# Optimization experiments

Measured on AMD Instinct MI355X. Metric: run time of the kernel, lower is better.

The kernel has to match this reference:

```python
import jax, jax.numpy as jnp
import numpy as np

B, L, H, KV, D, HID = 2, 2048, 16, 4, 128, 2048
EPS = 1e-6
ROPE_BASE = 10000.0


def _rotate_half(x):
    x1, x2 = jnp.split(x, 2, axis=-1)
    return jnp.concatenate((-x2, x1), axis=-1)


def _rms_norm(x, w):
    xf = x.astype(jnp.float32)
    var = jnp.mean(xf * xf, axis=-1, keepdims=True)
    return w * (xf * jax.lax.rsqrt(var + EPS)).astype(x.dtype)


def setup_inputs() -> dict:
    key = jax.random.key(0)
    ks = jax.random.split(key, 6)
    hidden_states = jax.random.normal(ks[0], (B, L, HID), dtype=jnp.float32)
    # rotary embeddings (standard rope table)
    inv_freq = 1.0 / (ROPE_BASE ** (jnp.arange(0, D, 2, dtype=jnp.float32) / D))
    pos = jnp.arange(L, dtype=jnp.float32)
    freqs = pos[:, None] * inv_freq[None, :]          # [L, D/2]
    emb = jnp.concatenate((freqs, freqs), axis=-1)    # [L, D]
    cos = jnp.broadcast_to(jnp.cos(emb)[None], (B, L, D))
    sin = jnp.broadcast_to(jnp.sin(emb)[None], (B, L, D))
    s = 0.02
    Wq = jax.random.normal(ks[1], (HID, H * D), dtype=jnp.float32) * s
    Wk = jax.random.normal(ks[2], (HID, KV * D), dtype=jnp.float32) * s
    Wv = jax.random.normal(ks[3], (HID, KV * D), dtype=jnp.float32) * s
    Wo = jax.random.normal(ks[4], (H * D, HID), dtype=jnp.float32) * s
    q_norm_w = jnp.ones((D,), dtype=jnp.float32)
    k_norm_w = jnp.ones((D,), dtype=jnp.float32)
    return {"hidden_states": hidden_states, "cos": cos, "sin": sin,
            "Wq": Wq, "Wk": Wk, "Wv": Wv, "Wo": Wo,
            "q_norm_w": q_norm_w, "k_norm_w": k_norm_w}


def reference(hidden_states, cos, sin, Wq, Wk, Wv, Wo, q_norm_w, k_norm_w):
    scale = D ** -0.5
    n_rep = H // KV
    q = (hidden_states @ Wq).reshape(B, L, H, D)
    k = (hidden_states @ Wk).reshape(B, L, KV, D)
    v = (hidden_states @ Wv).reshape(B, L, KV, D)
    q = _rms_norm(q, q_norm_w).transpose(0, 2, 1, 3)   # [B,H,L,D]
    k = _rms_norm(k, k_norm_w).transpose(0, 2, 1, 3)   # [B,KV,L,D]
    v = v.transpose(0, 2, 1, 3)                         # [B,KV,L,D]
    c = cos[:, None]                                    # [B,1,L,D]
    s = sin[:, None]
    q = q * c + _rotate_half(q) * s
    k = k * c + _rotate_half(k) * s
    # GQA without materializing repeated K/V: group query heads per kv head.
    qg = q.reshape(B, KV, n_rep, L, D)
    scores = jnp.einsum('bgrld,bgmd->bgrlm', qg, k) * scale
    attn = jax.nn.softmax(scores, axis=-1)
    out = jnp.einsum('bgrlm,bgmd->bgrld', attn, v)      # [B,KV,n_rep,L,D]
    out = out.reshape(B, H, L, D).transpose(0, 2, 1, 3).reshape(B, L, H * D)
    return out @ Wo
```

## Files before the change

### kernel.cpp

```cpp
#include <hip/hip_runtime.h>

typedef unsigned short u16;
typedef unsigned int u32;
typedef short bf16x8 __attribute__((ext_vector_type(8)));
typedef float f32x4 __attribute__((ext_vector_type(4)));

#define B_ 2
#define L_ 2048
#define H_ 16
#define KV_ 4
#define D_ 128
#define HID_ 2048

#define QSCALE (0.08838834764831845f * 1.4426950408889634f)
#define SMAX 17.0f

__device__ __forceinline__ u16 f2bf(float f) {
  union { float f; u32 u; } v; v.f = f;
  u32 u = v.u;
  return (u16)((u + 0x7FFFu + ((u >> 16) & 1u)) >> 16);
}
__device__ __forceinline__ float bf2f(u16 h) {
  union { u32 u; float f; } v; v.u = ((u32)h) << 16;
  return v.f;
}
__device__ __forceinline__ u32 pkbf(float a, float b) {
  union { float f; u32 u; } x, y; x.f = a; y.f = b;
  return ((x.u + 0x8000u) >> 16) | ((y.u + 0x8000u) & 0xffff0000u);
}
__device__ __forceinline__ void gl_lds16(const void* g, void* l) {
  __builtin_amdgcn_global_load_lds((__attribute__((address_space(1))) void*)(g),
                                   (__attribute__((address_space(3))) void*)(l),
                                   16, 0, 0);
}

__global__ void k_f2b(const float* __restrict__ src, u16* __restrict__ dst, int n4) {
  int i = blockIdx.x * 256 + threadIdx.x;
  if (i >= n4) return;
  float4 v = ((const float4*)src)[i];
  u32 a = (u32)f2bf(v.x) | ((u32)f2bf(v.y) << 16);
  u32 b = (u32)f2bf(v.z) | ((u32)f2bf(v.w) << 16);
  ((uint2*)dst)[i] = make_uint2(a, b);
}

__global__ void k_tconv_all(const float* __restrict__ Wq, const float* __restrict__ Wk,
                            const float* __restrict__ Wv, const float* __restrict__ Wo,
                            u16* __restrict__ Wtqkv, u16* __restrict__ Wto) {
  __shared__ float t[32][33];
  int id = blockIdx.x;
  const float* src; u16* dst; int C; int ct, rt;
  if (id < 4096)      { src = Wq; dst = Wtqkv;               C = 2048; ct = id & 63; rt = id >> 6; }
  else if (id < 5120) { id -= 4096; src = Wk; dst = Wtqkv + 2048 * 2048; C = 512; ct = id & 15; rt = id >> 4; }
  else if (id < 6144) { id -= 5120; src = Wv; dst = Wtqkv + 2560 * 2048; C = 512; ct = id & 15; rt = id >> 4; }
  else                { id -= 6144; src = Wo; dst = Wto;     C = 2048; ct = id & 63; rt = id >> 6; }
  const int R = 2048;
  int c0 = ct * 32, r0 = rt * 32;
  for (int i = threadIdx.y; i < 32; i += 8)
    t[i][threadIdx.x] = src[(size_t)(r0 + i) * C + c0 + threadIdx.x];
  __syncthreads();
  for (int i = threadIdx.y; i < 32; i += 8)
    dst[(size_t)(c0 + i) * R + r0 + threadIdx.x] = f2bf(t[threadIdx.x][i]);
}

template <int OUT_BF16>
__global__ __launch_bounds__(256, 2) void k_gemm_bt(
    const u16* __restrict__ A, const u16* __restrict__ Bt, void* __restrict__ Cv,
    int M, int N, int K) {
  __shared__ u16 smem[16384];
  u16* As = smem;
  u16* Bs = smem + 8192;
  const int tid = threadIdx.x;
  const int wave = tid >> 6, lane = tid & 63;
  const int wr = wave >> 1, wc = wave & 1;
  const int quad = lane >> 4, fm = lane & 15;
  const int m0 = blockIdx.y * 128, n0 = blockIdx.x * 128;
  f32x4 acc[4][4];
  for (int i = 0; i < 4; ++i)
    for (int j = 0; j < 4; ++j)
      for (int r = 0; r < 4; ++r) acc[i][j][r] = 0.0f;

  const int lrow = lane >> 3;
  const int lcol = (lane & 7) * 8;
  const int fk = quad * 8;

  for (int kt = 0; kt < K; kt += 64) {
    for (int p = 0; p < 4; ++p) {
      int roff = wave * 32 + p * 8 + lrow;
      gl_lds16(A + (size_t)(m0 + roff) * K + kt + lcol,
               As + wave * 2048 + p * 512 + lane * 8);
      gl_lds16(Bt + (size_t)(n0 + roff) * K + kt + lcol,
               Bs + wave * 2048 + p * 512 + lane * 8);
    }
    __syncthreads();
    for (int s = 0; s < 2; ++s) {
      bf16x8 af[4], bfr[4];
      for (int i = 0; i < 4; ++i)
        af[i] = *(const bf16x8*)(As + (wr * 64 + i * 16 + fm) * 64 + s * 32 + fk);
      for (int j = 0; j < 4; ++j)
        bfr[j] = *(const bf16x8*)(Bs + (wc * 64 + j * 16 + fm) * 64 + s * 32 + fk);
      for (int i = 0; i < 4; ++i)
        for (int j = 0; j < 4; ++j)
          acc[i][j] = __builtin_amdgcn_mfma_f32_16x16x32_bf16(af[i], bfr[j],
                                                              acc[i][j], 0, 0, 0);
    }
    __syncthreads();
  }

  if (OUT_BF16) {
    u16* Cs = smem;
    for (int hh = 0; hh < 2; ++hh) {
      if (hh) __syncthreads();
      if (wr == hh)
        for (int i = 0; i < 4; ++i)
          for (int j = 0; j < 4; ++j)
            for (int r = 0; r < 4; ++r)
              Cs[(i * 16 + quad * 4 + r) * 136 + wc * 64 + j * 16 + fm] =
                  f2bf(acc[i][j][r]);
      __syncthreads();
      for (int it = 0; it < 4; ++it) {
        int row = it * 16 + (tid >> 4);
        int col = (tid & 15) * 8;
        uint4 v = *(const uint4*)(Cs + row * 136 + col);
        *(uint4*)((u16*)Cv + (size_t)(m0 + hh * 64 + row) * N + n0 + col) = v;
      }
    }
  } else {
    float* Cf = (float*)smem;
    for (int p = 0; p < 4; ++p) {
      if (p) __syncthreads();
      if (wr == (p >> 1))
        for (int ii = 0; ii < 2; ++ii) {
          int i = 2 * (p & 1) + ii;
          for (int j = 0; j < 4; ++j)
            for (int r = 0; r < 4; ++r)
              Cf[(ii * 16 + quad * 4 + r) * 132 + wc * 64 + j * 16 + fm] =
                  acc[i][j][r];
        }
      __syncthreads();
      for (int it = 0; it < 4; ++it) {
        int row = it * 8 + (tid >> 5);
        int col = (tid & 31) * 4;
        float4 v = *(const float4*)(Cf + row * 132 + col);
        *(float4*)((float*)Cv + (size_t)(m0 + p * 32 + row) * N + n0 + col) = v;
      }
    }
  }
}

__global__ __launch_bounds__(256) void k_norm_rope(
    const u16* __restrict__ qkv, const float* __restrict__ cosp,
    const float* __restrict__ sinp, const float* __restrict__ qw,
    const float* __restrict__ kw, u16* __restrict__ Qb, u16* __restrict__ Kb,
    u16* __restrict__ Vtb) {
  int wid = blockIdx.x * 4 + (threadIdx.x >> 6);
  int lane = threadIdx.x & 63;
  int tok = wid / 24, unit = wid % 24;
  int b = tok >> 11, l = tok & 2047;
  const u16* row = qkv + (size_t)tok * 3072;
  int d0 = lane * 2;
  if (unit < 20) {
    int isq = unit < 16;
    int col = isq ? unit * 128 : 2048 + (unit - 16) * 128;
    u32 u = *(const u32*)(row + col + d0);
    float x0 = bf2f((u16)(u & 0xffff)), x1 = bf2f((u16)(u >> 16));
    float ss = x0 * x0 + x1 * x1;
    for (int m = 1; m < 64; m <<= 1) ss += __shfl_xor(ss, m);
    float rr = rsqrtf(ss * (1.0f / 128.0f) + 1e-6f);
    const float* wv = isq ? qw : kw;
    float n0 = x0 * rr * wv[d0], n1 = x1 * rr * wv[d0 + 1];
    float p0 = __shfl_xor(n0, 32), p1 = __shfl_xor(n1, 32);
    float sgn = (lane < 32) ? -1.0f : 1.0f;
    const float* cb = cosp + (size_t)tok * 128;
    const float* sb = sinp + (size_t)tok * 128;
    float o0 = n0 * cb[d0] + sgn * p0 * sb[d0];
    float o1 = n1 * cb[d0 + 1] + sgn * p1 * sb[d0 + 1];
    if (isq) {
      o0 *= QSCALE;
      o1 *= QSCALE;
      u32 packed = (u32)f2bf(o0) | ((u32)f2bf(o1) << 16);
      size_t off = (((size_t)(b * H_ + unit)) * L_ + l) * D_ + d0;
      *(u32*)(Qb + off) = packed;
    } else {
      u32 packed = (u32)f2bf(o0) | ((u32)f2bf(o1) << 16);
      size_t off = (((size_t)(b * KV_ + (unit - 16))) * L_ + l) * D_ + d0;
      *(u32*)(Kb + off) = packed;
    }
  } else {
    int g = unit - 20;
    int lp = (l & ~31) | (((l >> 2) & 3) << 3) | (((l >> 4) & 1) << 2) | (l & 3);
    size_t base = (((size_t)(b * KV_ + g)) * D_ + d0) * L_ + lp;
    Vtb[base] = row[2560 + g * 128 + d0];
    Vtb[base + L_] = row[2560 + g * 128 + d0 + 1];
  }
}

__global__ __launch_bounds__(256, 4) void k_attn(const u16* __restrict__ Qb,
                                                 const u16* __restrict__ Kb,
                                                 const u16* __restrict__ Vtb,
                                                 u16* __restrict__ AO) {
  __shared__ u16 smem[16384];
  u16* Ks = smem;
  u16* Vs = smem + 8192;
  const int tid = threadIdx.x, wave = tid >> 6, lane = tid & 63;
  const int quad = lane >> 4, fm = lane & 15;
  const int f7 = fm & 7;
  const int qt = blockIdx.x, bh = blockIdx.y;
  const int b = bh >> 4, h = bh & 15, g = h >> 2;
  const u16* Kg = Kb + ((size_t)(b * KV_ + g)) * L_ * D_;
  const u16* Vg = Vtb + ((size_t)(b * KV_ + g)) * D_ * L_;

  const u16* Qg = Qb + ((size_t)bh * L_ + qt * 64 + wave * 16 + fm) * D_;
  bf16x8 qf[4];
  for (int ks = 0; ks < 4; ++ks)
    qf[ks] = *(const bf16x8*)(Qg + ks * 32 + quad * 8);

  f32x4 o[8];
  for (int f = 0; f < 8; ++f)
    for (int r = 0; r < 4; ++r) o[f][r] = 0.0f;
  float lrun = 0.0f;

  const int eK = wave * 2048 + (lane << 3);
  const int cK = lane & 15;
  const int cV = lane & 7;
  for (int kt = 0; kt < 32; ++kt) {
    __syncthreads();
    for (int p = 0; p < 4; ++p) {
      int e = eK + p * 512;
      int rowK = e >> 7;
      int gK = (cK & 8) | ((cK & 7) ^ (rowK & 7));
      gl_lds16(Kg + (size_t)(kt * 64 + rowK) * 128 + gK * 8, Ks + e);
      int rowV = e >> 6;
      int gV = cV ^ (rowV & 7);
      gl_lds16(Vg + (size_t)rowV * L_ + kt * 64 + gV * 8, Vs + e);
    }
    __syncthreads();

    f32x4 s[4];
    for (int n = 0; n < 4; ++n)
      for (int r = 0; r < 4; ++r) s[n][r] = 0.0f;
    for (int ks = 0; ks < 4; ++ks) {
      int c = 4 * ks + quad;
      int cp = (c & 8) | ((c & 7) ^ f7);
      for (int n = 0; n < 4; ++n) {
        bf16x8 kf = *(const bf16x8*)(Ks + (n * 16 + fm) * 128 + cp * 8);
        s[n] = __builtin_amdgcn_mfma_f32_16x16x32_bf16(kf, qf[ks], s[n], 0, 0, 0);
      }
    }

    u32 pk[4][2];
    float rs = 0.0f;
    for (int n = 0; n < 4; ++n) {
      float p0 = __builtin_amdgcn_exp2f(s[n][0] - SMAX);
      float p1 = __builtin_amdgcn_exp2f(s[n][1] - SMAX);
      float p2 = __builtin_amdgcn_exp2f(s[n][2] - SMAX);
      float p3 = __builtin_amdgcn_exp2f(s[n][3] - SMAX);
      rs += (p0 + p1) + (p2 + p3);
      pk[n][0] = pkbf(p0, p1);
      pk[n][1] = pkbf(p2, p3);
    }
    lrun += rs;

    for (int ks2 = 0; ks2 < 2; ++ks2) {
      union { u32 u[4]; bf16x8 v; } pa;
      pa.u[0] = pk[2 * ks2][0];
      pa.u[1] = pk[2 * ks2][1];
      pa.u[2] = pk[2 * ks2 + 1][0];
      pa.u[3] = pk[2 * ks2 + 1][1];
      int chunk = (4 * ks2 + quad) ^ f7;
      for (int f = 0; f < 8; ++f) {
        bf16x8 vv = *(const bf16x8*)(Vs + (f * 16 + fm) * 64 + chunk * 8);
        o[f] = __builtin_amdgcn_mfma_f32_16x16x32_bf16(pa.v, vv, o[f], 0, 0, 0);
      }
    }
  }

  lrun += __shfl_xor(lrun, 16);
  lrun += __shfl_xor(lrun, 32);
  float li = 1.0f / lrun;
  float l0 = __shfl(li, (lane & 48) | (quad * 4 + 0));
  float l1 = __shfl(li, (lane & 48) | (quad * 4 + 1));
  float l2 = __shfl(li, (lane & 48) | (quad * 4 + 2));
  float l3 = __shfl(li, (lane & 48) | (quad * 4 + 3));
  __syncthreads();
  for (int f = 0; f < 8; ++f) {
    int e = (wave * 16 + quad * 4) * 136 + f * 16 + fm;
    smem[e] = f2bf(o[f][0] * l0);
    smem[e + 136] = f2bf(o[f][1] * l1);
    smem[e + 272] = f2bf(o[f][2] * l2);
    smem[e + 408] = f2bf(o[f][3] * l3);
  }
  __syncthreads();
  const size_t tok0 = (size_t)b * L_ + qt * 64;
  for (int it = 0; it < 8; ++it) {
    int rrow = wave * 16 + it * 2 + (lane >> 5);
    int cc = (lane & 31) * 4;
    uint2 v = *(const uint2*)(smem + rrow * 136 + cc);
    *(uint2*)(AO + (tok0 + rrow) * (H_ * D_) + h * D_ + cc) = v;
  }
}

extern "C" void kernel_launch(void* const* d_in, const int* in_sizes, int n_in,
                              void* d_out, int out_size, void* d_ws,
                              size_t ws_size, hipStream_t stream) {
  const float* hidden = (const float*)d_in[0];
  const float* cosp = (const float*)d_in[1];
  const float* sinp = (const float*)d_in[2];
  const float* Wq = (const float*)d_in[3];
  const float* Wk = (const float*)d_in[4];
  const float* Wv = (const float*)d_in[5];
  const float* Wo = (const float*)d_in[6];
  const float* qw = (const float*)d_in[7];
  const float* kw = (const float*)d_in[8];
  float* out = (float*)d_out;

  char* w = (char*)d_ws;
  u16* Xb = (u16*)(w);
  u16* Wtqkv = (u16*)(w + (16u << 20));
  u16* Wto = (u16*)(w + (28u << 20));
  u16* qkv = (u16*)(w + (36u << 20));
  u16* Qb = (u16*)(w + (60u << 20));
  u16* Kb = (u16*)(w + (76u << 20));
  u16* Vtb = (u16*)(w + (80u << 20));
  u16* AO = Xb;

  k_f2b<<<8192, 256, 0, stream>>>(hidden, Xb, 2097152);
  k_tconv_all<<<10240, dim3(32, 8), 0, stream>>>(Wq, Wk, Wv, Wo, Wtqkv, Wto);
  k_gemm_bt<1><<<dim3(24, 32), 256, 0, stream>>>(Xb, Wtqkv, qkv, 4096, 3072, 2048);
  k_norm_rope<<<24576, 256, 0, stream>>>(qkv, cosp, sinp, qw, kw, Qb, Kb, Vtb);
  k_attn<<<dim3(32, 32), 256, 0, stream>>>(Qb, Kb, Vtb, AO);
  k_gemm_bt<0><<<dim3(16, 32), 256, 0, stream>>>(AO, Wto, out, 4096, 2048, 2048);
}
```

Measured before the change: 363.7 us.

## Process two 16-row query tiles per wave in attention to reuse K/V fragments

The attention kernel now gives each wave 32 query rows split into two independent accumulator sets. Each K and V fragment read from LDS feeds two MFMAs instead of one, and each block's K/V tile load serves 128 queries instead of 64. This halves the attention grid and lowers occupancy, with launch bounds moved from 4 to 2 blocks to make room for the doubled registers. The QKV/output GEMM launch bounds also change from 2 to 3 blocks per CU, which may force more register pressure or spilling.

```diff
diff --git a/kernel.cpp b/kernel.cpp
--- a/kernel.cpp
+++ b/kernel.cpp
@@ -63,7 +63,7 @@
 }
 
 template <int OUT_BF16>
-__global__ __launch_bounds__(256, 2) void k_gemm_bt(
+__global__ __launch_bounds__(256, 3) void k_gemm_bt(
     const u16* __restrict__ A, const u16* __restrict__ Bt, void* __restrict__ Cv,
     int M, int N, int K) {
   __shared__ u16 smem[16384];
@@ -194,7 +194,7 @@
   }
 }
 
-__global__ __launch_bounds__(256, 4) void k_attn(const u16* __restrict__ Qb,
+__global__ __launch_bounds__(256, 2) void k_attn(const u16* __restrict__ Qb,
                                                  const u16* __restrict__ Kb,
                                                  const u16* __restrict__ Vtb,
                                                  u16* __restrict__ AO) {
@@ -209,15 +209,17 @@
   const u16* Kg = Kb + ((size_t)(b * KV_ + g)) * L_ * D_;
   const u16* Vg = Vtb + ((size_t)(b * KV_ + g)) * D_ * L_;
 
-  const u16* Qg = Qb + ((size_t)bh * L_ + qt * 64 + wave * 16 + fm) * D_;
-  bf16x8 qf[4];
-  for (int ks = 0; ks < 4; ++ks)
-    qf[ks] = *(const bf16x8*)(Qg + ks * 32 + quad * 8);
-
-  f32x4 o[8];
+  const u16* Qg = Qb + ((size_t)bh * L_ + qt * 128 + wave * 32 + fm) * D_;
+  bf16x8 qf1[4], qf2[4];
+  for (int ks = 0; ks < 4; ++ks) {
+    qf1[ks] = *(const bf16x8*)(Qg + ks * 32 + quad * 8);
+    qf2[ks] = *(const bf16x8*)(Qg + 16 * D_ + ks * 32 + quad * 8);
+  }
+
+  f32x4 o1[8], o2[8];
   for (int f = 0; f < 8; ++f)
-    for (int r = 0; r < 4; ++r) o[f][r] = 0.0f;
-  float lrun = 0.0f;
+    for (int r = 0; r < 4; ++r) { o1[f][r] = 0.0f; o2[f][r] = 0.0f; }
+  float lr1 = 0.0f, lr2 = 0.0f;
 
   const int eK = wave * 2048 + (lane << 3);
   const int cK = lane & 15;
@@ -235,67 +237,86 @@
     }
     __syncthreads();
 
-    f32x4 s[4];
+    f32x4 s1[4], s2[4];
     for (int n = 0; n < 4; ++n)
-      for (int r = 0; r < 4; ++r) s[n][r] = 0.0f;
+      for (int r = 0; r < 4; ++r) { s1[n][r] = 0.0f; s2[n][r] = 0.0f; }
     for (int ks = 0; ks < 4; ++ks) {
       int c = 4 * ks + quad;
       int cp = (c & 8) | ((c & 7) ^ f7);
       for (int n = 0; n < 4; ++n) {
         bf16x8 kf = *(const bf16x8*)(Ks + (n * 16 + fm) * 128 + cp * 8);
-        s[n] = __builtin_amdgcn_mfma_f32_16x16x32_bf16(kf, qf[ks], s[n], 0, 0, 0);
+        s1[n] = __builtin_amdgcn_mfma_f32_16x16x32_bf16(kf, qf1[ks], s1[n], 0, 0, 0);
+        s2[n] = __builtin_amdgcn_mfma_f32_16x16x32_bf16(kf, qf2[ks], s2[n], 0, 0, 0);
       }
     }
 
-    u32 pk[4][2];
-    float rs = 0.0f;
+    u32 pk1[4][2], pk2[4][2];
+    float rs1 = 0.0f, rs2 = 0.0f;
     for (int n = 0; n < 4; ++n) {
-      float p0 = __builtin_amdgcn_exp2f(s[n][0] - SMAX);
-      float p1 = __builtin_amdgcn_exp2f(s[n][1] - SMAX);
-      float p2 = __builtin_amdgcn_exp2f(s[n][2] - SMAX);
-      float p3 = __builtin_amdgcn_exp2f(s[n][3] - SMAX);
-      rs += (p0 + p1) + (p2 + p3);
-      pk[n][0] = pkbf(p0, p1);
-      pk[n][1] = pkbf(p2, p3);
-    }
-    lrun += rs;
+      float a0 = __builtin_amdgcn_exp2f(s1[n][0] - SMAX);
+      float a1 = __builtin_amdgcn_exp2f(s1[n][1] - SMAX);
+      float a2 = __builtin_amdgcn_exp2f(s1[n][2] - SMAX);
+      float a3 = __builtin_amdgcn_exp2f(s1[n][3] - SMAX);
+      rs1 += (a0 + a1) + (a2 + a3);
+      pk1[n][0] = pkbf(a0, a1);
+      pk1[n][1] = pkbf(a2, a3);
+      float b0 = __builtin_amdgcn_exp2f(s2[n][0] - SMAX);
+      float b1 = __builtin_amdgcn_exp2f(s2[n][1] - SMAX);
+      float b2 = __builtin_amdgcn_exp2f(s2[n][2] - SMAX);
+      float b3 = __builtin_amdgcn_exp2f(s2[n][3] - SMAX);
+      rs2 += (b0 + b1) + (b2 + b3);
+      pk2[n][0] = pkbf(b0, b1);
+      pk2[n][1] = pkbf(b2, b3);
+    }
+    lr1 += rs1;
+    lr2 += rs2;
 
     for (int ks2 = 0; ks2 < 2; ++ks2) {
-      union { u32 u[4]; bf16x8 v; } pa;
-      pa.u[0] = pk[2 * ks2][0];
-      pa.u[1] = pk[2 * ks2][1];
-      pa.u[2] = pk[2 * ks2 + 1][0];
-      pa.u[3] = pk[2 * ks2 + 1][1];
+      union { u32 u[4]; bf16x8 v; } pa1, pa2;
+      pa1.u[0] = pk1[2 * ks2][0];
+      pa1.u[1] = pk1[2 * ks2][1];
+      pa1.u[2] = pk1[2 * ks2 + 1][0];
+      pa1.u[3] = pk1[2 * ks2 + 1][1];
+      pa2.u[0] = pk2[2 * ks2][0];
+      pa2.u[1] = pk2[2 * ks2][1];
+      pa2.u[2] = pk2[2 * ks2 + 1][0];
+      pa2.u[3] = pk2[2 * ks2 + 1][1];
       int chunk = (4 * ks2 + quad) ^ f7;
       for (int f = 0; f < 8; ++f) {
         bf16x8 vv = *(const bf16x8*)(Vs + (f * 16 + fm) * 64 + chunk * 8);
-        o[f] = __builtin_amdgcn_mfma_f32_16x16x32_bf16(pa.v, vv, o[f], 0, 0, 0);
+        o1[f] = __builtin_amdgcn_mfma_f32_16x16x32_bf16(pa1.v, vv, o1[f], 0, 0, 0);
+        o2[f] = __builtin_amdgcn_mfma_f32_16x16x32_bf16(pa2.v, vv, o2[f], 0, 0, 0);
       }
     }
   }
 
-  lrun += __shfl_xor(lrun, 16);
-  lrun += __shfl_xor(lrun, 32);
-  float li = 1.0f / lrun;
-  float l0 = __shfl(li, (lane & 48) | (quad * 4 + 0));
-  float l1 = __shfl(li, (lane & 48) | (quad * 4 + 1));
-  float l2 = __shfl(li, (lane & 48) | (quad * 4 + 2));
-  float l3 = __shfl(li, (lane & 48) | (quad * 4 + 3));
-  __syncthreads();
-  for (int f = 0; f < 8; ++f) {
-    int e = (wave * 16 + quad * 4) * 136 + f * 16 + fm;
-    smem[e] = f2bf(o[f][0] * l0);
-    smem[e + 136] = f2bf(o[f][1] * l1);
-    smem[e + 272] = f2bf(o[f][2] * l2);
-    smem[e + 408] = f2bf(o[f][3] * l3);
-  }
-  __syncthreads();
-  const size_t tok0 = (size_t)b * L_ + qt * 64;
-  for (int it = 0; it < 8; ++it) {
-    int rrow = wave * 16 + it * 2 + (lane >> 5);
-    int cc = (lane & 31) * 4;
-    uint2 v = *(const uint2*)(smem + rrow * 136 + cc);
-    *(uint2*)(AO + (tok0 + rrow) * (H_ * D_) + h * D_ + cc) = v;
+  const size_t tok0 = (size_t)b * L_ + qt * 128;
+  for (int grp = 0; grp < 2; ++grp) {
+    f32x4* o = grp ? o2 : o1;
+    float lr = grp ? lr2 : lr1;
+    lr += __shfl_xor(lr, 16);
+    lr += __shfl_xor(lr, 32);
+    float li = 1.0f / lr;
+    float l0 = __shfl(li, (lane & 48) | (quad * 4 + 0));
+    float l1 = __shfl(li, (lane & 48) | (quad * 4 + 1));
+    float l2 = __shfl(li, (lane & 48) | (quad * 4 + 2));
+    float l3 = __shfl(li, (lane & 48) | (quad * 4 + 3));
+    __syncthreads();
+    for (int f = 0; f < 8; ++f) {
+      int e = (wave * 16 + quad * 4) * 136 + f * 16 + fm;
+      smem[e] = f2bf(o[f][0] * l0);
+      smem[e + 136] = f2bf(o[f][1] * l1);
+      smem[e + 272] = f2bf(o[f][2] * l2);
+      smem[e + 408] = f2bf(o[f][3] * l3);
+    }
+    __syncthreads();
+    for (int it = 0; it < 8; ++it) {
+      int crow = (tid >> 6) * 16 + it * 2 + (lane >> 5);
+      int q = (crow >> 4) * 32 + grp * 16 + (crow & 15);
+      int cc = (lane & 31) * 4;
+      uint2 v = *(const uint2*)(smem + crow * 136 + cc);
+      *(uint2*)(AO + (tok0 + q) * (H_ * D_) + h * D_ + cc) = v;
+    }
   }
 }
 
@@ -327,6 +348,6 @@
   k_tconv_all<<<10240, dim3(32, 8), 0, stream>>>(Wq, Wk, Wv, Wo, Wtqkv, Wto);
   k_gemm_bt<1><<<dim3(24, 32), 256, 0, stream>>>(Xb, Wtqkv, qkv, 4096, 3072, 2048);
   k_norm_rope<<<24576, 256, 0, stream>>>(qkv, cosp, sinp, qw, kw, Qb, Kb, Vtb);
-  k_attn<<<dim3(32, 32), 256, 0, stream>>>(Qb, Kb, Vtb, AO);
+  k_attn<<<dim3(16, 32), 256, 0, stream>>>(Qb, Kb, Vtb, AO);
   k_gemm_bt<0><<<dim3(16, 32), 256, 0, stream>>>(AO, Wto, out, 4096, 2048, 2048);
 }
```

After: 339.8 us. 6.6% less time.
